# Kernel optimization log

Measured on AMD Instinct MI355X. Metric: run time of the kernel, lower is better.

The kernel has to match this reference:

```python
import jax, jax.numpy as jnp
import numpy as np

N = 8192
IN_F = 64
OUT_F = 64
D_INT = 32
ALPHA = 0.2  # LeakyReLU negative slope


def setup_inputs() -> dict:
    key = jax.random.key(0)
    k1, k2, k3, k4 = jax.random.split(key, 4)
    x = jax.random.normal(k1, (N, IN_F), dtype=jnp.float32)
    adj = jnp.ones((N, N), dtype=bool)  # unused by the original forward math
    intent_embeds = jax.random.normal(k2, (N, D_INT), dtype=jnp.float32)
    # Xavier-uniform-like init scales (gain 1.414)
    limW = 1.414 * np.sqrt(6.0 / (IN_F + OUT_F))
    W = jax.random.uniform(k3, (IN_F, OUT_F), dtype=jnp.float32, minval=-limW, maxval=limW)
    a_len = 2 * OUT_F + 2 * D_INT
    lima = 1.414 * np.sqrt(6.0 / (a_len + 1))
    a = jax.random.uniform(k4, (a_len, 1), dtype=jnp.float32, minval=-lima, maxval=lima)
    return {"input": x, "adj": adj, "intent_embeds": intent_embeds, "W": W, "a": a}


def reference(input, adj, intent_embeds, W, a):
    # h: [N, F]
    h = input @ W
    F_ = h.shape[1]
    a = a[:, 0]
    a_src, a_dst = a[:F_], a[F_:2 * F_]
    b_src, b_dst = a[2 * F_:2 * F_ + D_INT], a[2 * F_ + D_INT:]
    # Additive score decomposes exactly: e[i,j] = lrelu(s_i + t_j)
    s = h @ a_src + intent_embeds @ b_src          # [N]
    t = h @ a_dst + intent_embeds @ b_dst          # [N]
    e = jax.nn.leaky_relu(s[:, None] + t[None, :], negative_slope=ALPHA)  # [N, N]
    # NOTE: original applies softmax over dim=0 (source axis), no adj masking
    attention = jax.nn.softmax(e, axis=0)
    h_prime = attention @ h                        # [N, F]
    return jax.nn.elu(h_prime)
```

## Files before the change

kernel.cpp:

```cpp
#include <hip/hip_runtime.h>
#include <cstdint>
#include <cstddef>

#define N_NODES 8192
#define F_OUT   64
#define DINT    32
#define ALPHA   0.2f

__global__ __launch_bounds__(64) void k_h_st(
    const float* __restrict__ x, const float* __restrict__ ie,
    const float* __restrict__ W, const float* __restrict__ a,
    float* __restrict__ h, float* __restrict__ s, float* __restrict__ t)
{
    const int i = blockIdx.x;
    const int f = threadIdx.x;
    const float* xr = x + (size_t)i * 64;

    float acc = 0.f;
    #pragma unroll 16
    for (int k = 0; k < 64; ++k)
        acc = fmaf(xr[k], W[k * 64 + f], acc);

    h[(size_t)i * 64 + f] = acc;

    float ps = acc * a[f];
    float pt = acc * a[64 + f];
    if (f < DINT) {
        float e = ie[(size_t)i * DINT + f];
        ps = fmaf(e, a[128 + f], ps);
        pt = fmaf(e, a[160 + f], pt);
    }
    #pragma unroll
    for (int m = 1; m < 64; m <<= 1) {
        ps += __shfl_xor(ps, m, 64);
        pt += __shfl_xor(pt, m, 64);
    }
    if (f == 0) { s[i] = ps; t[i] = pt; }
}

__global__ __launch_bounds__(256) void k_ranks(
    const float* __restrict__ s, const float* __restrict__ t,
    float* __restrict__ smax,
    int* __restrict__ pos, int* __restrict__ inv_t,
    float* __restrict__ t_sorted, int* __restrict__ q_sorted,
    float* __restrict__ se1, float* __restrict__ se2)
{
    __shared__ __align__(16) float s_sh[2048];
    __shared__ __align__(16) float t_sh[2048];
    const int wave = threadIdx.x >> 6, lane = threadIdx.x & 63;
    const int idx = blockIdx.x * 4 + wave;
    const int which = blockIdx.y;

    const float key = (which == 0) ? s[idx] : t[idx];
    const float nkey = -key;
    int c1 = 0, c2 = 0;
    float m = -1e30f;

    for (int c = 0; c < 4; ++c) {
        const int base = c * 2048;
        #pragma unroll
        for (int l = 0; l < 2; ++l) {
            int o = threadIdx.x * 4 + l * 1024;
            *reinterpret_cast<float4*>(&s_sh[o]) =
                *reinterpret_cast<const float4*>(&s[base + o]);
            *reinterpret_cast<float4*>(&t_sh[o]) =
                *reinterpret_cast<const float4*>(&t[base + o]);
        }
        __syncthreads();

        if (which == 0) {
            for (int k = lane * 4; k < 2048; k += 256) {
                float4 sv = *reinterpret_cast<const float4*>(&s_sh[k]);
                float4 tv = *reinterpret_cast<const float4*>(&t_sh[k]);
                const int k0 = base + k;
                c1 += (sv.x < key) || (sv.x == key && (k0 + 0) < idx);
                c1 += (sv.y < key) || (sv.y == key && (k0 + 1) < idx);
                c1 += (sv.z < key) || (sv.z == key && (k0 + 2) < idx);
                c1 += (sv.w < key) || (sv.w == key && (k0 + 3) < idx);
                c2 += (tv.x < nkey) + (tv.y < nkey) + (tv.z < nkey) + (tv.w < nkey);
                m = fmaxf(m, fmaxf(fmaxf(sv.x, sv.y), fmaxf(sv.z, sv.w)));
            }
        } else {
            for (int k = lane * 4; k < 2048; k += 256) {
                float4 tv = *reinterpret_cast<const float4*>(&t_sh[k]);
                float4 sv = *reinterpret_cast<const float4*>(&s_sh[k]);
                const int k0 = base + k;
                c1 += (tv.x < key) || (tv.x == key && (k0 + 0) < idx);
                c1 += (tv.y < key) || (tv.y == key && (k0 + 1) < idx);
                c1 += (tv.z < key) || (tv.z == key && (k0 + 2) < idx);
                c1 += (tv.w < key) || (tv.w == key && (k0 + 3) < idx);
                c2 += (sv.x < nkey) + (sv.y < nkey) + (sv.z < nkey) + (sv.w < nkey);
            }
        }
        __syncthreads();
    }

    int p = c1 * 16384 + c2;
    #pragma unroll
    for (int mm = 1; mm < 64; mm <<= 1) p += __shfl_xor(p, mm, 64);

    if (which == 0) {
        #pragma unroll
        for (int mm = 1; mm < 64; mm <<= 1) m = fmaxf(m, __shfl_xor(m, mm, 64));
        if (lane == 0) {
            const int r1 = p >> 14, r2 = p & 16383;
            pos[idx] = r2;
            const float d = key - m;
            se1[r1] = __expf(d);
            se2[r1] = __expf(ALPHA * d);
            if (idx == 0) smax[0] = m;
        }
    } else if (lane == 0) {
        const int r1 = p >> 14, r2 = p & 16383;
        inv_t[r1] = idx;
        t_sorted[r1] = key;
        q_sorted[r1] = r2;
    }
}

__global__ __launch_bounds__(1024) void k_mid(
    const float* __restrict__ se1, const float* __restrict__ se2,
    const float* __restrict__ smax_p,
    const float* __restrict__ t_sorted, const int* __restrict__ q_sorted,
    float* __restrict__ SufP1, float* __restrict__ PreP2,
    float* __restrict__ cf1, float* __restrict__ cf2)
{
    __shared__ double sc[1024];
    const int tid = threadIdx.x;
    double loc[8], sum;

    sum = 0.0;
    #pragma unroll
    for (int k = 0; k < 8; ++k) { loc[k] = (double)se2[tid * 8 + k]; sum += loc[k]; }
    sc[tid] = sum; __syncthreads();
    for (int off = 1; off < 1024; off <<= 1) {
        double v = (tid >= off) ? sc[tid - off] : 0.0;
        __syncthreads();
        sc[tid] += v;
        __syncthreads();
    }
    {
        double run = sc[tid] - sum;
        #pragma unroll
        for (int k = 0; k < 8; ++k) { PreP2[tid * 8 + k] = (float)run; run += loc[k]; }
        if (tid == 1023) PreP2[8192] = (float)run;
    }
    __syncthreads();

    sum = 0.0;
    #pragma unroll
    for (int k = 0; k < 8; ++k) { loc[k] = (double)se1[tid * 8 + k]; sum += loc[k]; }
    sc[tid] = sum; __syncthreads();
    for (int off = 1; off < 1024; off <<= 1) {
        double v = (tid >= off) ? sc[tid - off] : 0.0;
        __syncthreads();
        sc[tid] += v;
        __syncthreads();
    }
    {
        double acc = sc[1023] - sc[tid];
        #pragma unroll
        for (int k = 7; k >= 0; --k) { acc += loc[k]; SufP1[tid * 8 + k] = (float)acc; }
        if (tid == 1023) SufP1[8192] = 0.f;
    }

    __threadfence();
    __syncthreads();

    const float smax = smax_p[0];
    #pragma unroll
    for (int k = 0; k < 8; ++k) {
        const int r = tid + k * 1024;
        const float tj = t_sorted[r];
        const float zc = smax + tj;
        const float c = fmaxf(zc, ALPHA * zc);
        const float E1 = __expf(zc - c);
        const float E2 = __expf(ALPHA * zc - c);
        const int qj = q_sorted[r];
        const float D = E1 * SufP1[qj] + E2 * PreP2[qj];
        const float invD = 1.f / D;
        cf1[r] = E1 * invD;
        cf2[r] = E2 * invD;
    }
}

__global__ __launch_bounds__(256) void k_tilesum(
    const float* __restrict__ h, const int* __restrict__ inv_t,
    const float* __restrict__ cf1, const float* __restrict__ cf2,
    float* __restrict__ T1, float* __restrict__ T2)
{
    const int tile = blockIdx.x;
    const int wave = threadIdx.x >> 6, f = threadIdx.x & 63;
    const int r0 = tile * 128 + wave * 32;
    float a1 = 0.f, a2 = 0.f;
    for (int k = 0; k < 32; ++k) {
        const int r = r0 + k;
        const int j = inv_t[r];
        const float v = h[(size_t)j * 64 + f];
        a1 = fmaf(cf1[r], v, a1);
        a2 = fmaf(cf2[r], v, a2);
    }
    __shared__ float red[2][4][64];
    red[0][wave][f] = a1; red[1][wave][f] = a2;
    __syncthreads();
    if (wave == 0)
        T1[tile * 64 + f] = red[0][0][f] + red[0][1][f] + red[0][2][f] + red[0][3][f];
    else if (wave == 1)
        T2[tile * 64 + f] = red[1][0][f] + red[1][1][f] + red[1][2][f] + red[1][3][f];
}

__global__ __launch_bounds__(64) void k_scan2(
    const float* __restrict__ h, const int* __restrict__ inv_t,
    const float* __restrict__ cf1, const float* __restrict__ cf2,
    const float* __restrict__ T1, const float* __restrict__ T2,
    float* __restrict__ S1, float* __restrict__ S2)
{
    const int tile = blockIdx.x, arr = blockIdx.y, f = threadIdx.x;
    if (arr == 0) {
        float acc = 0.f;
        for (int tt = tile + 1; tt < 64; ++tt) acc += T1[tt * 64 + f];
        if (tile == 63) S1[(size_t)8192 * 64 + f] = 0.f;
        for (int rb = 15; rb >= 0; --rb) {
            const int r0 = tile * 128 + rb * 8;
            float v[8];
            #pragma unroll
            for (int k = 0; k < 8; ++k)
                v[k] = cf1[r0 + k] * h[(size_t)inv_t[r0 + k] * 64 + f];
            #pragma unroll
            for (int k = 7; k >= 0; --k) { acc += v[k]; S1[(size_t)(r0 + k) * 64 + f] = acc; }
        }
    } else {
        float acc = 0.f;
        for (int tt = 0; tt < tile; ++tt) acc += T2[tt * 64 + f];
        for (int rb = 0; rb < 16; ++rb) {
            const int r0 = tile * 128 + rb * 8;
            float v[8];
            #pragma unroll
            for (int k = 0; k < 8; ++k)
                v[k] = cf2[r0 + k] * h[(size_t)inv_t[r0 + k] * 64 + f];
            #pragma unroll
            for (int k = 0; k < 8; ++k) { S2[(size_t)(r0 + k) * 64 + f] = acc; acc += v[k]; }
        }
        if (tile == 63) S2[(size_t)8192 * 64 + f] = acc;
    }
}

__global__ __launch_bounds__(256) void k_out(
    const float* __restrict__ s, const float* __restrict__ smax_p,
    const int* __restrict__ pos,
    const float* __restrict__ S1, const float* __restrict__ S2,
    float* __restrict__ out)
{
    const int i = blockIdx.x * 4 + (threadIdx.x >> 6);
    const int f = threadIdx.x & 63;
    const float d = s[i] - smax_p[0];
    const float e1 = __expf(d), e2 = __expf(ALPHA * d);
    const int p = pos[i];
    const float v = fmaf(e1, S1[(size_t)p * 64 + f], e2 * S2[(size_t)p * 64 + f]);
    out[(size_t)i * 64 + f] = v > 0.f ? v : expm1f(v);
}

extern "C" void kernel_launch(void* const* d_in, const int* in_sizes, int n_in,
                              void* d_out, int out_size, void* d_ws, size_t ws_size,
                              hipStream_t stream)
{
    const float* x  = (const float*)d_in[0];
    const float* ie = (const float*)d_in[2];
    const float* W  = (const float*)d_in[3];
    const float* a  = (const float*)d_in[4];
    float* out = (float*)d_out;

    float* p = (float*)d_ws;
    float* h        = p; p += (size_t)N_NODES * F_OUT;
    float* s        = p; p += N_NODES;
    float* t        = p; p += N_NODES;
    float* smax     = p; p += 16;
    float* se1      = p; p += N_NODES;
    float* se2      = p; p += N_NODES;
    float* SufP1    = p; p += N_NODES + 64;
    float* PreP2    = p; p += N_NODES + 64;
    float* t_sorted = p; p += N_NODES;
    float* cf1      = p; p += N_NODES;
    float* cf2      = p; p += N_NODES;
    float* T1       = p; p += 64 * 64;
    float* T2       = p; p += 64 * 64;
    float* S1       = p; p += (size_t)(N_NODES + 1) * F_OUT + 64;
    float* S2       = p; p += (size_t)(N_NODES + 1) * F_OUT + 64;
    int* pos        = (int*)p; p += N_NODES;
    int* inv_t      = (int*)p; p += N_NODES;
    int* q_sorted   = (int*)p; p += N_NODES;

    k_h_st    <<<N_NODES, 64, 0, stream>>>(x, ie, W, a, h, s, t);
    k_ranks   <<<dim3(N_NODES / 4, 2), 256, 0, stream>>>(s, t, smax,
                      pos, inv_t, t_sorted, q_sorted, se1, se2);
    k_mid     <<<1, 1024, 0, stream>>>(se1, se2, smax, t_sorted, q_sorted,
                      SufP1, PreP2, cf1, cf2);
    k_tilesum <<<64, 256, 0, stream>>>(h, inv_t, cf1, cf2, T1, T2);
    k_scan2   <<<dim3(64, 2), 64, 0, stream>>>(h, inv_t, cf1, cf2, T1, T2, S1, S2);
    k_out     <<<N_NODES / 4, 256, 0, stream>>>(s, smax, pos, S1, S2, out);
}
```

Measured before the change: 385.8 us.

## Rank eight keys per wave with packed u64 keys and wave-scan the midpoint

The rank kernel now has each wave rank eight keys instead of one. Each shared-memory element is loaded once and compared against all eight keys, and the sign-flipped float bits are packed with the index into a single 64-bit key, so the tie-break becomes one compare. This cuts LDS traffic and block count by 8x. The single-block k_mid replaces its two double-precision Hillis-Steele LDS scans, which needed many barriers, with shuffle-based wave scans plus a cross-wave reduction, and it keeps the prefix and suffix tables in shared memory instead of global. The cost is more registers per thread and 64-bit compares.

```diff
diff --git a/kernel.cpp b/kernel.cpp
--- a/kernel.cpp
+++ b/kernel.cpp
@@ -45,76 +45,110 @@
     float* __restrict__ t_sorted, int* __restrict__ q_sorted,
     float* __restrict__ se1, float* __restrict__ se2)
 {
-    __shared__ __align__(16) float s_sh[2048];
-    __shared__ __align__(16) float t_sh[2048];
+    __shared__ __align__(16) unsigned long long u_sh[2048];
+    __shared__ __align__(16) float f_sh[2048];
     const int wave = threadIdx.x >> 6, lane = threadIdx.x & 63;
-    const int idx = blockIdx.x * 4 + wave;
     const int which = blockIdx.y;
-
-    const float key = (which == 0) ? s[idx] : t[idx];
-    const float nkey = -key;
-    int c1 = 0, c2 = 0;
-    float m = -1e30f;
+    const int key0 = blockIdx.x * 32 + wave * 8;
+
+    const float* __restrict__ karr = (which == 0) ? s : t;
+    const float* __restrict__ oarr = (which == 0) ? t : s;
+
+    float kf[8], nk[8];
+    unsigned long long ku[8];
+    #pragma unroll
+    for (int l = 0; l < 8; ++l) {
+        kf[l] = karr[key0 + l];
+        unsigned int b = __float_as_uint(kf[l]);
+        b = (b & 0x80000000u) ? ~b : (b | 0x80000000u);
+        ku[l] = ((unsigned long long)b << 32) | (unsigned int)(key0 + l);
+        nk[l] = -kf[l];
+    }
+
+    int c1[8] = {0,0,0,0,0,0,0,0}, c2[8] = {0,0,0,0,0,0,0,0};
+    unsigned long long mx = 0ull;
 
     for (int c = 0; c < 4; ++c) {
         const int base = c * 2048;
+        {
+            const int e0 = threadIdx.x * 8;
+            float4 a0 = *reinterpret_cast<const float4*>(&karr[base + e0]);
+            float4 a1 = *reinterpret_cast<const float4*>(&karr[base + e0 + 4]);
+            float4 b0 = *reinterpret_cast<const float4*>(&oarr[base + e0]);
+            float4 b1 = *reinterpret_cast<const float4*>(&oarr[base + e0 + 4]);
+            const float av[8] = {a0.x,a0.y,a0.z,a0.w,a1.x,a1.y,a1.z,a1.w};
+            #pragma unroll
+            for (int e = 0; e < 8; ++e) {
+                unsigned int b = __float_as_uint(av[e]);
+                b = (b & 0x80000000u) ? ~b : (b | 0x80000000u);
+                u_sh[e0 + e] = ((unsigned long long)b << 32)
+                             | (unsigned int)(base + e0 + e);
+            }
+            *reinterpret_cast<float4*>(&f_sh[e0])     = b0;
+            *reinterpret_cast<float4*>(&f_sh[e0 + 4]) = b1;
+        }
+        __syncthreads();
+
+        for (int k = lane * 4; k < 2048; k += 256) {
+            const ulonglong2 p0 = *reinterpret_cast<const ulonglong2*>(&u_sh[k]);
+            const ulonglong2 p1 = *reinterpret_cast<const ulonglong2*>(&u_sh[k + 2]);
+            const float4 fv = *reinterpret_cast<const float4*>(&f_sh[k]);
+            if (which == 0) {
+                unsigned long long m01 = p0.x > p0.y ? p0.x : p0.y;
+                unsigned long long m23 = p1.x > p1.y ? p1.x : p1.y;
+                unsigned long long m03 = m01 > m23 ? m01 : m23;
+                mx = mx > m03 ? mx : m03;
+            }
+            #pragma unroll
+            for (int l = 0; l < 8; ++l) {
+                c1[l] += (int)(p0.x < ku[l]) + (int)(p0.y < ku[l])
+                       + (int)(p1.x < ku[l]) + (int)(p1.y < ku[l]);
+                c2[l] += (int)(fv.x < nk[l]) + (int)(fv.y < nk[l])
+                       + (int)(fv.z < nk[l]) + (int)(fv.w < nk[l]);
+            }
+        }
+        __syncthreads();
+    }
+
+    int pk[8];
+    #pragma unroll
+    for (int l = 0; l < 8; ++l) pk[l] = c1[l] * 16384 + c2[l];
+    #pragma unroll
+    for (int m = 1; m < 64; m <<= 1) {
         #pragma unroll
-        for (int l = 0; l < 2; ++l) {
-            int o = threadIdx.x * 4 + l * 1024;
-            *reinterpret_cast<float4*>(&s_sh[o]) =
-                *reinterpret_cast<const float4*>(&s[base + o]);
-            *reinterpret_cast<float4*>(&t_sh[o]) =
-                *reinterpret_cast<const float4*>(&t[base + o]);
-        }
-        __syncthreads();
-
-        if (which == 0) {
-            for (int k = lane * 4; k < 2048; k += 256) {
-                float4 sv = *reinterpret_cast<const float4*>(&s_sh[k]);
-                float4 tv = *reinterpret_cast<const float4*>(&t_sh[k]);
-                const int k0 = base + k;
-                c1 += (sv.x < key) || (sv.x == key && (k0 + 0) < idx);
-                c1 += (sv.y < key) || (sv.y == key && (k0 + 1) < idx);
-                c1 += (sv.z < key) || (sv.z == key && (k0 + 2) < idx);
-                c1 += (sv.w < key) || (sv.w == key && (k0 + 3) < idx);
-                c2 += (tv.x < nkey) + (tv.y < nkey) + (tv.z < nkey) + (tv.w < nkey);
-                m = fmaxf(m, fmaxf(fmaxf(sv.x, sv.y), fmaxf(sv.z, sv.w)));
-            }
-        } else {
-            for (int k = lane * 4; k < 2048; k += 256) {
-                float4 tv = *reinterpret_cast<const float4*>(&t_sh[k]);
-                float4 sv = *reinterpret_cast<const float4*>(&s_sh[k]);
-                const int k0 = base + k;
-                c1 += (tv.x < key) || (tv.x == key && (k0 + 0) < idx);
-                c1 += (tv.y < key) || (tv.y == key && (k0 + 1) < idx);
-                c1 += (tv.z < key) || (tv.z == key && (k0 + 2) < idx);
-                c1 += (tv.w < key) || (tv.w == key && (k0 + 3) < idx);
-                c2 += (sv.x < nkey) + (sv.y < nkey) + (sv.z < nkey) + (sv.w < nkey);
-            }
-        }
-        __syncthreads();
-    }
-
-    int p = c1 * 16384 + c2;
-    #pragma unroll
-    for (int mm = 1; mm < 64; mm <<= 1) p += __shfl_xor(p, mm, 64);
+        for (int l = 0; l < 8; ++l) pk[l] += __shfl_xor(pk[l], m, 64);
+    }
 
     if (which == 0) {
         #pragma unroll
-        for (int mm = 1; mm < 64; mm <<= 1) m = fmaxf(m, __shfl_xor(m, mm, 64));
+        for (int m = 1; m < 64; m <<= 1) {
+            unsigned long long o = __shfl_xor(mx, m, 64);
+            mx = mx > o ? mx : o;
+        }
         if (lane == 0) {
-            const int r1 = p >> 14, r2 = p & 16383;
-            pos[idx] = r2;
-            const float d = key - m;
-            se1[r1] = __expf(d);
-            se2[r1] = __expf(ALPHA * d);
-            if (idx == 0) smax[0] = m;
+            unsigned int b = (unsigned int)(mx >> 32);
+            b = (b & 0x80000000u) ? (b ^ 0x80000000u) : ~b;
+            const float smax_f = __uint_as_float(b);
+            if (key0 == 0) smax[0] = smax_f;
+            #pragma unroll
+            for (int l = 0; l < 8; ++l) {
+                const int idx = key0 + l;
+                const int r1 = pk[l] >> 14, r2 = pk[l] & 16383;
+                pos[idx] = r2;
+                const float d = kf[l] - smax_f;
+                se1[r1] = __expf(d);
+                se2[r1] = __expf(ALPHA * d);
+            }
         }
     } else if (lane == 0) {
-        const int r1 = p >> 14, r2 = p & 16383;
-        inv_t[r1] = idx;
-        t_sorted[r1] = key;
-        q_sorted[r1] = r2;
+        #pragma unroll
+        for (int l = 0; l < 8; ++l) {
+            const int idx = key0 + l;
+            const int r1 = pk[l] >> 14, r2 = pk[l] & 16383;
+            inv_t[r1] = idx;
+            t_sorted[r1] = kf[l];
+            q_sorted[r1] = r2;
+        }
     }
 }
 
@@ -122,49 +156,44 @@
     const float* __restrict__ se1, const float* __restrict__ se2,
     const float* __restrict__ smax_p,
     const float* __restrict__ t_sorted, const int* __restrict__ q_sorted,
-    float* __restrict__ SufP1, float* __restrict__ PreP2,
     float* __restrict__ cf1, float* __restrict__ cf2)
 {
-    __shared__ double sc[1024];
-    const int tid = threadIdx.x;
-    double loc[8], sum;
-
-    sum = 0.0;
-    #pragma unroll
-    for (int k = 0; k < 8; ++k) { loc[k] = (double)se2[tid * 8 + k]; sum += loc[k]; }
-    sc[tid] = sum; __syncthreads();
-    for (int off = 1; off < 1024; off <<= 1) {
-        double v = (tid >= off) ? sc[tid - off] : 0.0;
-        __syncthreads();
-        sc[tid] += v;
-        __syncthreads();
-    }
-    {
-        double run = sc[tid] - sum;
-        #pragma unroll
-        for (int k = 0; k < 8; ++k) { PreP2[tid * 8 + k] = (float)run; run += loc[k]; }
-        if (tid == 1023) PreP2[8192] = (float)run;
-    }
+    __shared__ float suf1[8200];
+    __shared__ float pre2[8200];
+    __shared__ double wred[2][16];
+    const int tid = threadIdx.x, wave = tid >> 6, lane = tid & 63;
+    const int base = tid * 8;
+
+    double l1[8], l2[8], s1 = 0.0, s2 = 0.0;
+    #pragma unroll
+    for (int k = 0; k < 8; ++k) {
+        l1[k] = (double)se1[base + k]; s1 += l1[k];
+        l2[k] = (double)se2[base + k]; s2 += l2[k];
+    }
+    double i1 = s1, i2 = s2;
+    #pragma unroll
+    for (int off = 1; off < 64; off <<= 1) {
+        double v1 = __shfl_up(i1, off, 64);
+        double v2 = __shfl_up(i2, off, 64);
+        if (lane >= off) { i1 += v1; i2 += v2; }
+    }
+    if (lane == 63) { wred[0][wave] = i1; wred[1][wave] = i2; }
     __syncthreads();
-
-    sum = 0.0;
-    #pragma unroll
-    for (int k = 0; k < 8; ++k) { loc[k] = (double)se1[tid * 8 + k]; sum += loc[k]; }
-    sc[tid] = sum; __syncthreads();
-    for (int off = 1; off < 1024; off <<= 1) {
-        double v = (tid >= off) ? sc[tid - off] : 0.0;
-        __syncthreads();
-        sc[tid] += v;
-        __syncthreads();
-    }
-    {
-        double acc = sc[1023] - sc[tid];
-        #pragma unroll
-        for (int k = 7; k >= 0; --k) { acc += loc[k]; SufP1[tid * 8 + k] = (float)acc; }
-        if (tid == 1023) SufP1[8192] = 0.f;
-    }
-
-    __threadfence();
+    double off1 = 0, off2 = 0, tot1 = 0, tot2 = 0;
+    #pragma unroll
+    for (int w = 0; w < 16; ++w) {
+        const double a = wred[0][w], b = wred[1][w];
+        if (w < wave) { off1 += a; off2 += b; }
+        tot1 += a; tot2 += b;
+    }
+    double run1 = off1 + (i1 - s1);
+    double run2 = off2 + (i2 - s2);
+    #pragma unroll
+    for (int k = 0; k < 8; ++k) {
+        suf1[base + k] = (float)(tot1 - run1); run1 += l1[k];
+        pre2[base + k] = (float)run2;          run2 += l2[k];
+    }
+    if (tid == 1023) { suf1[8192] = 0.f; pre2[8192] = (float)tot2; }
     __syncthreads();
 
     const float smax = smax_p[0];
@@ -177,7 +206,7 @@
         const float E1 = __expf(zc - c);
         const float E2 = __expf(ALPHA * zc - c);
         const int qj = q_sorted[r];
-        const float D = E1 * SufP1[qj] + E2 * PreP2[qj];
+        const float D = E1 * suf1[qj] + E2 * pre2[qj];
         const float invD = 1.f / D;
         cf1[r] = E1 * invD;
         cf2[r] = E2 * invD;
@@ -277,8 +306,6 @@
     float* smax     = p; p += 16;
     float* se1      = p; p += N_NODES;
     float* se2      = p; p += N_NODES;
-    float* SufP1    = p; p += N_NODES + 64;
-    float* PreP2    = p; p += N_NODES + 64;
     float* t_sorted = p; p += N_NODES;
     float* cf1      = p; p += N_NODES;
     float* cf2      = p; p += N_NODES;
@@ -291,10 +318,10 @@
     int* q_sorted   = (int*)p; p += N_NODES;
 
     k_h_st    <<<N_NODES, 64, 0, stream>>>(x, ie, W, a, h, s, t);
-    k_ranks   <<<dim3(N_NODES / 4, 2), 256, 0, stream>>>(s, t, smax,
+    k_ranks   <<<dim3(N_NODES / 32, 2), 256, 0, stream>>>(s, t, smax,
                       pos, inv_t, t_sorted, q_sorted, se1, se2);
     k_mid     <<<1, 1024, 0, stream>>>(se1, se2, smax, t_sorted, q_sorted,
-                      SufP1, PreP2, cf1, cf2);
+                      cf1, cf2);
     k_tilesum <<<64, 256, 0, stream>>>(h, inv_t, cf1, cf2, T1, T2);
     k_scan2   <<<dim3(64, 2), 64, 0, stream>>>(h, inv_t, cf1, cf2, T1, T2, S1, S2);
     k_out     <<<N_NODES / 4, 256, 0, stream>>>(s, smax, pos, S1, S2, out);
```

Measured after the change: 362.5 us. -6.0%, faster.
